# Optimization experiments

Hardware: AMD Instinct MI355X
Metric: run time of the kernel (lower is better)

## Reference

```python
import jax, jax.numpy as jnp
import numpy as np

B, H, W = 4, 180, 180
C_L, C_C, C_OUT = 128, 128, 256
CH_ALL = 2 * (C_L + C_C)        # 512
CH_HID = CH_ALL // 3            # 170


def setup_inputs() -> dict:
    key = jax.random.key(0)
    ks = jax.random.split(key, 12)
    N = 160000
    inp = {
        'lidar_features': jax.random.normal(ks[0], (N, C_L), dtype=jnp.float32),
        'img_bev': jax.random.normal(ks[1], (B, C_C, H, W), dtype=jnp.float32),
        'batch_idx': jnp.sort(jax.random.randint(ks[2], (N,), 0, B, dtype=jnp.int32)),
        'y_idx': jax.random.randint(ks[3], (N,), 0, H, dtype=jnp.int32),
        'x_idx': jax.random.randint(ks[4], (N,), 0, W, dtype=jnp.int32),
        # weights stored as [in, out] (x @ W), equivalent to torch Linear weight.T
        'Wl1': jax.random.normal(ks[5], (CH_ALL, CH_HID), dtype=jnp.float32) * 0.02,
        'Wl2': jax.random.normal(ks[6], (CH_HID, C_L), dtype=jnp.float32) * 0.02,
        'Wc1': jax.random.normal(ks[7], (CH_ALL, CH_HID), dtype=jnp.float32) * 0.02,
        'Wc2': jax.random.normal(ks[8], (CH_HID, C_C), dtype=jnp.float32) * 0.02,
        'Wf1': jax.random.normal(ks[9], (C_L + C_C, C_OUT), dtype=jnp.float32) * 0.02,
        'Wf2': jax.random.normal(ks[10], (C_OUT, C_OUT), dtype=jnp.float32) * 0.02,
    }
    return inp


def reference(lidar_features, img_bev, Wl1, Wl2, Wc1, Wc2, Wf1, Wf2,
              batch_idx, y_idx, x_idx):
    relu = jax.nn.relu
    spatial_size = H * W
    # flatten dense image BEV map: [B,C,H,W] -> [B*H*W, C]
    img_flat = jnp.transpose(img_bev, (0, 2, 3, 1)).reshape(B * H * W, C_C)
    # per-voxel flat row index (faithful to original incl. clamp to spatial_size-2)
    row = batch_idx * spatial_size + y_idx * W + x_idx
    row = jnp.clip(row, 0, spatial_size - 2)
    cam_feat = img_flat[row]                                  # [N, C_C] gather
    # per-batch segment min/max (ragged reduction)
    lmin = jax.ops.segment_min(lidar_features, batch_idx, num_segments=B)
    lmax = jax.ops.segment_max(lidar_features, batch_idx, num_segments=B)
    cmin = jax.ops.segment_min(cam_feat, batch_idx, num_segments=B)
    cmax = jax.ops.segment_max(cam_feat, batch_idx, num_segments=B)
    cat_mm = jnp.concatenate([lmin, lmax, cmin, cmax], axis=-1)   # [B, 512]
    att_l = jax.nn.sigmoid(relu(relu(cat_mm @ Wl1) @ Wl2))        # [B, C_L]
    att_c = jax.nn.sigmoid(relu(relu(cat_mm @ Wc1) @ Wc2))        # [B, C_C]
    gated_l = lidar_features * att_l[batch_idx]
    gated_c = cam_feat * att_c[batch_idx]
    fused = jnp.concatenate([gated_l, gated_c], axis=-1)          # [N, 256]
    out = relu(relu(fused @ Wf1) @ Wf2)                           # [N, 256]
    return out
```

## Files before the change

kernel.cpp:

```cpp
#include <hip/hip_runtime.h>
#include <math.h>

#define NB 4
#define HH 180
#define WWW 180
#define SPATIAL (HH*WWW)
#define CH_HID 170
#define CLAMP_ROW (SPATIAL-2)

typedef short v8s __attribute__((ext_vector_type(8)));
typedef short v4s __attribute__((ext_vector_type(4)));
typedef float v4f __attribute__((ext_vector_type(4)));

__device__ __forceinline__ unsigned fmap(float f) {
    unsigned u = __float_as_uint(f);
    return (u & 0x80000000u) ? ~u : (u | 0x80000000u);
}
__device__ __forceinline__ float funmap(unsigned u) {
    unsigned b = (u & 0x80000000u) ? (u & 0x7FFFFFFFu) : ~u;
    return __uint_as_float(b);
}
__device__ __forceinline__ unsigned short f2bf(float f) {
    unsigned u = __float_as_uint(f);
    u += 0x7FFFu + ((u >> 16) & 1);
    return (unsigned short)(u >> 16);
}

__global__ void k_prep(const float* __restrict__ Wf1, const float* __restrict__ Wf2,
                       unsigned short* __restrict__ W1T, unsigned short* __restrict__ W2T) {
    const float* W = blockIdx.y ? Wf2 : Wf1;
    unsigned short* WT = blockIdx.y ? W2T : W1T;
    __shared__ float t[32][33];
    int bx = blockIdx.x & 7, by = blockIdx.x >> 3;
    int lx = threadIdx.x & 31, ly = threadIdx.x >> 5;
    for (int i = 0; i < 4; ++i)
        t[ly + i*8][lx] = W[(by*32 + ly + i*8)*256 + bx*32 + lx];
    __syncthreads();
    for (int i = 0; i < 4; ++i)
        WT[(bx*32 + ly + i*8)*256 + by*32 + lx] = f2bf(t[lx][ly + i*8]);
}

__global__ void k_setup(const float* __restrict__ img, float* __restrict__ camT,
                        unsigned* __restrict__ stats) {
    if (blockIdx.y == 0 && blockIdx.x < 8) {
        int i = blockIdx.x * 256 + threadIdx.x;
        int j = i & 511;
        bool is_min = (j < 128) || (j >= 256 && j < 384);
        stats[i] = is_min ? 0xFFFFFFFFu : 0u;
    }
    __shared__ float tile[32][33];
    int s0 = blockIdx.x * 32, c0 = blockIdx.y * 32;
    int lx = threadIdx.x & 31, ly = threadIdx.x >> 5;
    for (int i = 0; i < 4; ++i) {
        int s = s0 + lx;
        if (s < SPATIAL)
            tile[ly + i*8][lx] = img[(c0 + ly + i*8) * SPATIAL + s];
    }
    __syncthreads();
    for (int i = 0; i < 4; ++i) {
        int s = s0 + ly + i*8;
        if (s < SPATIAL)
            camT[s*128 + c0 + lx] = tile[lx][ly + i*8];
    }
}

__global__ __launch_bounds__(256)
void k_reduce(const float* __restrict__ lidar, const float* __restrict__ camT,
              const int* __restrict__ bidx, const int* __restrict__ yidx,
              const int* __restrict__ xidx,
              unsigned* __restrict__ stats, int N, int chunk) {
    __shared__ int sb[256];
    __shared__ int srow[256];
    __shared__ v4f redmn[4][64];
    __shared__ v4f redmx[4][64];
    const int tid = threadIdx.x;
    const int vbeg = blockIdx.x * chunk;
    const int cnt = min(chunk, N - vbeg);
    if (cnt <= 0) return;
    if (tid < cnt) {
        int v = vbeg + tid;
        sb[tid] = bidx[v];
        srow[tid] = min(yidx[v]*WWW + xidx[v] + sb[tid]*SPATIAL, CLAMP_ROW);
    }
    __syncthreads();

    const int sub = tid >> 6;
    const int lane = tid & 63;
    const int c4 = lane * 4;
    const bool cam = (c4 >= 128);
    const int cc = cam ? (c4 - 128) : c4;
    const int min_off = cam ? (c4 + 128) : c4;

    const int b_first = sb[0], b_last = sb[cnt - 1];
    int s0 = 0;
    for (int bb = b_first; bb <= b_last; ++bb) {
        int s1 = cnt;
        if (bb < b_last) {
            int lo = s0, hi = cnt;
            while (lo < hi) { int mid = (lo + hi) >> 1; if (sb[mid] > bb) hi = mid; else lo = mid + 1; }
            s1 = lo;
        }
        float mn0 = INFINITY, mn1 = INFINITY, mn2 = INFINITY, mn3 = INFINITY;
        float mx0 = -INFINITY, mx1 = -INFINITY, mx2 = -INFINITY, mx3 = -INFINITY;
        const bool skipload = cam && (bb > 0);
        if (!skipload) {
            #pragma unroll 4
            for (int idx = s0 + sub; idx < s1; idx += 4) {
                const float* src = cam ? &camT[(size_t)srow[idx]*128 + cc]
                                       : &lidar[(size_t)(vbeg + idx)*128 + c4];
                v4f val = *(const v4f*)src;
                mn0 = fminf(mn0, val[0]); mx0 = fmaxf(mx0, val[0]);
                mn1 = fminf(mn1, val[1]); mx1 = fmaxf(mx1, val[1]);
                mn2 = fminf(mn2, val[2]); mx2 = fmaxf(mx2, val[2]);
                mn3 = fminf(mn3, val[3]); mx3 = fmaxf(mx3, val[3]);
            }
        } else {
            v4f cv = *(const v4f*)&camT[(size_t)CLAMP_ROW*128 + cc];
            mn0 = mx0 = cv[0]; mn1 = mx1 = cv[1]; mn2 = mx2 = cv[2]; mn3 = mx3 = cv[3];
        }
        redmn[sub][lane] = (v4f){mn0, mn1, mn2, mn3};
        redmx[sub][lane] = (v4f){mx0, mx1, mx2, mx3};
        __syncthreads();
        if (sub == 0) {
            v4f a0 = redmn[0][lane], a1 = redmn[1][lane], a2 = redmn[2][lane], a3 = redmn[3][lane];
            v4f b0 = redmx[0][lane], b1 = redmx[1][lane], b2 = redmx[2][lane], b3 = redmx[3][lane];
            int base = bb*512 + min_off;
            for (int j = 0; j < 4; ++j) {
                float mn = fminf(fminf(a0[j], a1[j]), fminf(a2[j], a3[j]));
                float mx = fmaxf(fmaxf(b0[j], b1[j]), fmaxf(b2[j], b3[j]));
                atomicMin(&stats[base + j], fmap(mn));
                atomicMax(&stats[base + 128 + j], fmap(mx));
            }
        }
        __syncthreads();
        s0 = s1;
    }
}

__global__ void k_mlp(const unsigned* __restrict__ stats,
                      const float* __restrict__ Wl1, const float* __restrict__ Wl2,
                      const float* __restrict__ Wc1, const float* __restrict__ Wc2,
                      float* __restrict__ att) {
    __shared__ float cat[512];
    __shared__ float hid[CH_HID];
    int b = blockIdx.x >> 1;
    int net = blockIdx.x & 1;
    const float* W1 = net ? Wc1 : Wl1;
    const float* W2 = net ? Wc2 : Wl2;
    int tid = threadIdx.x;
    for (int j = tid; j < 512; j += 256) cat[j] = funmap(stats[b*512 + j]);
    __syncthreads();
    if (tid < CH_HID) {
        float s = 0.f;
        for (int k = 0; k < 512; ++k) s += cat[k] * W1[k*CH_HID + tid];
        hid[tid] = fmaxf(s, 0.f);
    }
    __syncthreads();
    if (tid < 128) {
        float s = 0.f;
        for (int k = 0; k < CH_HID; ++k) s += hid[k] * W2[k*128 + tid];
        s = fmaxf(s, 0.f);
        att[b*256 + net*128 + tid] = 1.f / (1.f + expf(-s));
    }
}

__global__ __launch_bounds__(256, 3)
void k_main(const float* __restrict__ lidar, const float* __restrict__ camT,
            const int* __restrict__ bidx, const int* __restrict__ yidx,
            const int* __restrict__ xidx, const float* __restrict__ att,
            const unsigned short* __restrict__ W1T, const unsigned short* __restrict__ W2T,
            float* __restrict__ out, int N) {
    __shared__ __align__(16) unsigned short sA[64][264];
    __shared__ float satt[NB*256];
    __shared__ int srow[64];
    __shared__ int sbb[64];
    const int tid = threadIdx.x;
    const int v0 = blockIdx.x * 64;

    for (int i = 0; i < 4; ++i) satt[i*256 + tid] = att[i*256 + tid];
    if (tid < 64) {
        int v = v0 + tid;
        int b = 0, row = 0;
        if (v < N) {
            b = bidx[v];
            row = min(b*SPATIAL + yidx[v]*WWW + xidx[v], CLAMP_ROW);
        }
        sbb[tid] = b;
        srow[tid] = row;
    }
    __syncthreads();

    {
        const int c = (tid & 63) * 4;
        const bool cam = (c >= 128);
        for (int j = 0; j < 16; ++j) {
            int m = j*4 + (tid >> 6);
            int v = v0 + m;
            v4f val = {0.f, 0.f, 0.f, 0.f};
            if (v < N) {
                int b = sbb[m];
                const float* src = cam ? &camT[(size_t)srow[m]*128 + (c - 128)]
                                       : &lidar[(size_t)v*128 + c];
                v4f x = *(const v4f*)src;
                for (int jj = 0; jj < 4; ++jj)
                    val[jj] = x[jj] * satt[b*256 + c + jj];
            }
            v4s pk;
            for (int jj = 0; jj < 4; ++jj) pk[jj] = (short)f2bf(val[jj]);
            *(v4s*)&sA[m][c] = pk;
        }
    }

    const int wave = tid >> 6;
    const int lane = tid & 63;
    const int ml = lane & 15;
    const int q = lane >> 4;

    for (int layer = 0; layer < 2; ++layer) {
        const unsigned short* WT = layer ? W2T : W1T;
        v4f acc[4][4];
        const v4f zz = {0.f, 0.f, 0.f, 0.f};
        for (int rt = 0; rt < 4; ++rt)
            for (int ct = 0; ct < 4; ++ct) acc[rt][ct] = zz;

        __syncthreads();
        const unsigned short* wb = WT + (size_t)(wave*64 + ml)*256 + q*8;
        #pragma unroll
        for (int ks = 0; ks < 8; ++ks) {
            v8s a[4];
            const int ka = ks*32 + q*8;
            for (int rt = 0; rt < 4; ++rt)
                a[rt] = *(const v8s*)&sA[rt*16 + ml][ka];
            for (int ct = 0; ct < 4; ++ct) {
                v8s bfr = *(const v8s*)&wb[ct*16*256 + ks*32];
                for (int rt = 0; rt < 4; ++rt)
                    acc[rt][ct] = __builtin_amdgcn_mfma_f32_16x16x32_bf16(
                        a[rt], bfr, acc[rt][ct], 0, 0, 0);
            }
        }
        __syncthreads();
        if (layer == 0) {
            for (int rt = 0; rt < 4; ++rt)
                for (int ct = 0; ct < 4; ++ct)
                    for (int r = 0; r < 4; ++r)
                        sA[rt*16 + q*4 + r][wave*64 + ct*16 + ml] =
                            f2bf(fmaxf(acc[rt][ct][r], 0.f));
        } else {
            for (int rt = 0; rt < 4; ++rt)
                for (int ct = 0; ct < 4; ++ct) {
                    const int col = wave*64 + ct*16 + ml;
                    for (int r = 0; r < 4; ++r) {
                        int v = v0 + rt*16 + q*4 + r;
                        if (v < N) out[(size_t)v*256 + col] = fmaxf(acc[rt][ct][r], 0.f);
                    }
                }
        }
    }
}

extern "C" void kernel_launch(void* const* d_in, const int* in_sizes, int n_in,
                              void* d_out, int out_size, void* d_ws, size_t ws_size,
                              hipStream_t stream) {
    const float* lidar = (const float*)d_in[0];
    const float* img   = (const float*)d_in[1];
    const int*   bidx  = (const int*)d_in[2];
    const int*   yidx  = (const int*)d_in[3];
    const int*   xidx  = (const int*)d_in[4];
    const float* Wl1   = (const float*)d_in[5];
    const float* Wl2   = (const float*)d_in[6];
    const float* Wc1   = (const float*)d_in[7];
    const float* Wc2   = (const float*)d_in[8];
    const float* Wf1   = (const float*)d_in[9];
    const float* Wf2   = (const float*)d_in[10];
    float* out = (float*)d_out;
    const int N = in_sizes[0] / 128;

    unsigned* stats = (unsigned*)d_ws;
    float* att = (float*)((char*)d_ws + 8192);
    unsigned short* W1T = (unsigned short*)((char*)d_ws + 16384);
    unsigned short* W2T = (unsigned short*)((char*)d_ws + 16384 + 131072);
    float* camT = (float*)((char*)d_ws + 16384 + 262144);

    k_prep<<<dim3(64, 2), 256, 0, stream>>>(Wf1, Wf2, W1T, W2T);
    k_setup<<<dim3((SPATIAL + 31) / 32, 4), 256, 0, stream>>>(img, camT, stats);
    const int rblocks = 1280;
    const int chunk = (N + rblocks - 1) / rblocks;
    k_reduce<<<rblocks, 256, 0, stream>>>(lidar, camT, bidx, yidx, xidx, stats, N, chunk);
    k_mlp<<<8, 256, 0, stream>>>(stats, Wl1, Wl2, Wc1, Wc2, att);
    k_main<<<(N + 63) / 64, 256, 0, stream>>>(lidar, camT, bidx, yidx, xidx, att, W1T, W2T, out, N);
}
```

Measured before the change: 467.5 us.

## Pre-swizzle weights into MFMA fragment order, stage output through LDS, batch gathers

Weight preparation now writes Wf1/Wf2 directly in per-lane MFMA B-fragment order, so each lane loads one contiguous 16-byte chunk instead of strided rows. The stats init moves into k_prep. The gather loop issues eight independent loads before any arithmetic and reads attention from registers selected by batch instead of LDS. The final layer output goes through LDS so global stores become coalesced 16-byte row writes rather than scattered 4-byte writes. The reduce grid is doubled and the small MLP loops are unrolled. The cost is higher register pressure and extra barriers.

New measurement: 443.4 us. -5.2%, faster.

```diff
diff --git a/kernel.cpp b/kernel.cpp
--- a/kernel.cpp
+++ b/kernel.cpp
@@ -27,27 +27,29 @@
 }
 
 __global__ void k_prep(const float* __restrict__ Wf1, const float* __restrict__ Wf2,
-                       unsigned short* __restrict__ W1T, unsigned short* __restrict__ W2T) {
-    const float* W = blockIdx.y ? Wf2 : Wf1;
-    unsigned short* WT = blockIdx.y ? W2T : W1T;
-    __shared__ float t[32][33];
-    int bx = blockIdx.x & 7, by = blockIdx.x >> 3;
-    int lx = threadIdx.x & 31, ly = threadIdx.x >> 5;
-    for (int i = 0; i < 4; ++i)
-        t[ly + i*8][lx] = W[(by*32 + ly + i*8)*256 + bx*32 + lx];
-    __syncthreads();
-    for (int i = 0; i < 4; ++i)
-        WT[(bx*32 + ly + i*8)*256 + by*32 + lx] = f2bf(t[lx][ly + i*8]);
-}
-
-__global__ void k_setup(const float* __restrict__ img, float* __restrict__ camT,
-                        unsigned* __restrict__ stats) {
+                       unsigned short* __restrict__ W1S, unsigned short* __restrict__ W2S,
+                       unsigned* __restrict__ stats) {
     if (blockIdx.y == 0 && blockIdx.x < 8) {
         int i = blockIdx.x * 256 + threadIdx.x;
         int j = i & 511;
         bool is_min = (j < 128) || (j >= 256 && j < 384);
         stats[i] = is_min ? 0xFFFFFFFFu : 0u;
     }
+    const float* W = blockIdx.y ? Wf2 : Wf1;
+    unsigned short* WS = blockIdx.y ? W2S : W1S;
+    const int tid = threadIdx.x;
+    const int frag = blockIdx.x * 4 + (tid >> 6);
+    const int lane = tid & 63;
+    const int nt = frag >> 3, ks = frag & 7;
+    const int q = lane >> 4, ml = lane & 15;
+    v8s pk;
+    #pragma unroll
+    for (int j = 0; j < 8; ++j)
+        pk[j] = (short)f2bf(W[(ks*32 + q*8 + j)*256 + nt*16 + ml]);
+    *(v8s*)&WS[(frag*64 + lane)*8] = pk;
+}
+
+__global__ void k_setup(const float* __restrict__ img, float* __restrict__ camT) {
     __shared__ float tile[32][33];
     int s0 = blockIdx.x * 32, c0 = blockIdx.y * 32;
     int lx = threadIdx.x & 31, ly = threadIdx.x >> 5;
@@ -152,12 +154,14 @@
     __syncthreads();
     if (tid < CH_HID) {
         float s = 0.f;
+        #pragma unroll 16
         for (int k = 0; k < 512; ++k) s += cat[k] * W1[k*CH_HID + tid];
         hid[tid] = fmaxf(s, 0.f);
     }
     __syncthreads();
     if (tid < 128) {
         float s = 0.f;
+        #pragma unroll 10
         for (int k = 0; k < CH_HID; ++k) s += hid[k] * W2[k*128 + tid];
         s = fmaxf(s, 0.f);
         att[b*256 + net*128 + tid] = 1.f / (1.f + expf(-s));
@@ -168,16 +172,16 @@
 void k_main(const float* __restrict__ lidar, const float* __restrict__ camT,
             const int* __restrict__ bidx, const int* __restrict__ yidx,
             const int* __restrict__ xidx, const float* __restrict__ att,
-            const unsigned short* __restrict__ W1T, const unsigned short* __restrict__ W2T,
+            const unsigned short* __restrict__ W1S, const unsigned short* __restrict__ W2S,
             float* __restrict__ out, int N) {
-    __shared__ __align__(16) unsigned short sA[64][264];
-    __shared__ float satt[NB*256];
+    __shared__ __align__(16) char smem[64 * 264 * 2];
+    unsigned short (*sA)[264] = (unsigned short(*)[264])smem;
+    float* sAf = (float*)smem;
     __shared__ int srow[64];
     __shared__ int sbb[64];
     const int tid = threadIdx.x;
     const int v0 = blockIdx.x * 64;
 
-    for (int i = 0; i < 4; ++i) satt[i*256 + tid] = att[i*256 + tid];
     if (tid < 64) {
         int v = v0 + tid;
         int b = 0, row = 0;
@@ -188,24 +192,37 @@
         sbb[tid] = b;
         srow[tid] = row;
     }
-    __syncthreads();
-
-    {
-        const int c = (tid & 63) * 4;
-        const bool cam = (c >= 128);
-        for (int j = 0; j < 16; ++j) {
-            int m = j*4 + (tid >> 6);
-            int v = v0 + m;
-            v4f val = {0.f, 0.f, 0.f, 0.f};
-            if (v < N) {
-                int b = sbb[m];
-                const float* src = cam ? &camT[(size_t)srow[m]*128 + (c - 128)]
-                                       : &lidar[(size_t)v*128 + c];
-                v4f x = *(const v4f*)src;
-                for (int jj = 0; jj < 4; ++jj)
-                    val[jj] = x[jj] * satt[b*256 + c + jj];
-            }
+    const int c = (tid & 63) * 4;
+    const bool cam = (c >= 128);
+    v4f attv0 = *(const v4f*)&att[0*256 + c];
+    v4f attv1 = *(const v4f*)&att[1*256 + c];
+    v4f attv2 = *(const v4f*)&att[2*256 + c];
+    v4f attv3 = *(const v4f*)&att[3*256 + c];
+    __syncthreads();
+
+    #pragma unroll
+    for (int half = 0; half < 2; ++half) {
+        v4f x[8]; int bm[8];
+        #pragma unroll
+        for (int j = 0; j < 8; ++j) {
+            int m = (half*8 + j)*4 + (tid >> 6);
+            int vc = min(v0 + m, N - 1);
+            bm[j] = sbb[m];
+            const float* src = cam ? &camT[(size_t)srow[m]*128 + (c - 128)]
+                                   : &lidar[(size_t)vc*128 + c];
+            x[j] = *(const v4f*)src;
+        }
+        #pragma unroll
+        for (int j = 0; j < 8; ++j) {
+            int m = (half*8 + j)*4 + (tid >> 6);
+            int b = bm[j];
+            v4f a = attv0;
+            if (b == 1) a = attv1;
+            if (b == 2) a = attv2;
+            if (b == 3) a = attv3;
+            v4f val = x[j] * a;
             v4s pk;
+            #pragma unroll
             for (int jj = 0; jj < 4; ++jj) pk[jj] = (short)f2bf(val[jj]);
             *(v4s*)&sA[m][c] = pk;
         }
@@ -216,23 +233,25 @@
     const int ml = lane & 15;
     const int q = lane >> 4;
 
+    v4f acc[4][4];
     for (int layer = 0; layer < 2; ++layer) {
-        const unsigned short* WT = layer ? W2T : W1T;
-        v4f acc[4][4];
+        const unsigned short* WS = layer ? W2S : W1S;
         const v4f zz = {0.f, 0.f, 0.f, 0.f};
         for (int rt = 0; rt < 4; ++rt)
             for (int ct = 0; ct < 4; ++ct) acc[rt][ct] = zz;
 
         __syncthreads();
-        const unsigned short* wb = WT + (size_t)(wave*64 + ml)*256 + q*8;
         #pragma unroll
         for (int ks = 0; ks < 8; ++ks) {
             v8s a[4];
             const int ka = ks*32 + q*8;
+            #pragma unroll
             for (int rt = 0; rt < 4; ++rt)
                 a[rt] = *(const v8s*)&sA[rt*16 + ml][ka];
+            #pragma unroll
             for (int ct = 0; ct < 4; ++ct) {
-                v8s bfr = *(const v8s*)&wb[ct*16*256 + ks*32];
+                v8s bfr = *(const v8s*)&WS[(((wave*4 + ct)*8 + ks)*64 + lane)*8];
+                #pragma unroll
                 for (int rt = 0; rt < 4; ++rt)
                     acc[rt][ct] = __builtin_amdgcn_mfma_f32_16x16x32_bf16(
                         a[rt], bfr, acc[rt][ct], 0, 0, 0);
@@ -245,15 +264,26 @@
                     for (int r = 0; r < 4; ++r)
                         sA[rt*16 + q*4 + r][wave*64 + ct*16 + ml] =
                             f2bf(fmaxf(acc[rt][ct][r], 0.f));
-        } else {
-            for (int rt = 0; rt < 4; ++rt)
-                for (int ct = 0; ct < 4; ++ct) {
-                    const int col = wave*64 + ct*16 + ml;
-                    for (int r = 0; r < 4; ++r) {
-                        int v = v0 + rt*16 + q*4 + r;
-                        if (v < N) out[(size_t)v*256 + col] = fmaxf(acc[rt][ct][r], 0.f);
-                    }
-                }
+        }
+    }
+
+    const int c4 = (tid & 63) * 4;
+    #pragma unroll
+    for (int p = 0; p < 2; ++p) {
+        __syncthreads();
+        #pragma unroll
+        for (int rt = 2*p; rt < 2*p + 2; ++rt)
+            for (int ct = 0; ct < 4; ++ct)
+                for (int r = 0; r < 4; ++r)
+                    sAf[((rt - 2*p)*16 + q*4 + r)*260 + wave*64 + ct*16 + ml] =
+                        fmaxf(acc[rt][ct][r], 0.f);
+        __syncthreads();
+        #pragma unroll
+        for (int i = 0; i < 8; ++i) {
+            int rl = (tid >> 6) + i*4;
+            int v = v0 + p*32 + rl;
+            if (v < N)
+                *(v4f*)&out[(size_t)v*256 + c4] = *(const v4f*)&sAf[rl*260 + c4];
         }
     }
 }
@@ -277,15 +307,15 @@
 
     unsigned* stats = (unsigned*)d_ws;
     float* att = (float*)((char*)d_ws + 8192);
-    unsigned short* W1T = (unsigned short*)((char*)d_ws + 16384);
-    unsigned short* W2T = (unsigned short*)((char*)d_ws + 16384 + 131072);
+    unsigned short* W1S = (unsigned short*)((char*)d_ws + 16384);
+    unsigned short* W2S = (unsigned short*)((char*)d_ws + 16384 + 131072);
     float* camT = (float*)((char*)d_ws + 16384 + 262144);
 
-    k_prep<<<dim3(64, 2), 256, 0, stream>>>(Wf1, Wf2, W1T, W2T);
-    k_setup<<<dim3((SPATIAL + 31) / 32, 4), 256, 0, stream>>>(img, camT, stats);
-    const int rblocks = 1280;
+    k_prep<<<dim3(32, 2), 256, 0, stream>>>(Wf1, Wf2, W1S, W2S, stats);
+    k_setup<<<dim3((SPATIAL + 31) / 32, 4), 256, 0, stream>>>(img, camT);
+    const int rblocks = 2560;
     const int chunk = (N + rblocks - 1) / rblocks;
     k_reduce<<<rblocks, 256, 0, stream>>>(lidar, camT, bidx, yidx, xidx, stats, N, chunk);
     k_mlp<<<8, 256, 0, stream>>>(stats, Wl1, Wl2, Wc1, Wc2, att);
-    k_main<<<(N + 63) / 64, 256, 0, stream>>>(lidar, camT, bidx, yidx, xidx, att, W1T, W2T, out, N);
-}
+    k_main<<<(N + 63) / 64, 256, 0, stream>>>(lidar, camT, bidx, yidx, xidx, att, W1S, W2S, out, N);
+}
```
